# Optimization experiments

Measured on AMD Instinct MI355X. Metric: run time of the kernel, lower is better.

## Reference

```python
import jax, jax.numpy as jnp
import numpy as np

B, C, D = 4096, 1000, 3072


def setup_inputs() -> dict:
    key = jax.random.key(0)
    k1, k2, k3, k4 = jax.random.split(key, 4)
    scale = 1.0
    return {
        "z": jax.random.normal(k1, (B, D), dtype=jnp.float32),
        "sldj": jax.random.normal(k2, (B,), dtype=jnp.float32),
        "labels": jax.random.randint(k3, (B,), 0, C),
        "beta": jnp.ones((), dtype=jnp.float32),
        "means": jax.random.normal(k4, (C, D), dtype=jnp.float32) * scale,
    }


def reference(z, sldj, labels, beta, means):
    # dists[i,j] = -0.5 * ||z_i - mu_j||^2, via a^2 + b^2 - 2ab GEMM trick
    z2 = jnp.sum(z * z, axis=1, keepdims=True)          # [B,1]
    m2 = jnp.sum(means * means, axis=1)[None, :]        # [1,C]
    cross = jnp.einsum('bd,cd->bc', z, means)           # [B,C] GEMM
    dists = -0.5 * (z2 + m2 - 2.0 * cross)              # [B,C]

    log_pz = jax.nn.logsumexp(dists, axis=1)            # [B]
    # cross_entropy(dists, labels) = mean(logsumexp - dists[i, y_i])
    picked = jnp.take_along_axis(dists, labels[:, None], axis=1)[:, 0]
    loss_cls = jnp.mean(log_pz - picked)
    loss_gen = -jnp.mean(log_pz + sldj) / z.shape[1]
    total = loss_gen + beta * loss_cls
    return total, loss_gen, loss_cls
```

## Files before the change

### kernel.cpp

```cpp
#include <hip/hip_runtime.h>
#include <hip/hip_bf16.h>
#include <cstdint>
#include <cstddef>

#define NB 4096
#define NC 1000
#define NCP 1024
#define ND 3072
#define NSL 4
#define KSL (ND / NSL)
#define BM 256
#define BN 256
#define BK 32
#define NT (KSL / BK)
#define ABUF (BM * BK)
#define BBUF (BN * BK)

typedef __attribute__((ext_vector_type(8))) __bf16 bf16x8;
typedef __attribute__((ext_vector_type(4))) float f32x4;
typedef __attribute__((ext_vector_type(4))) unsigned short u16x4;
typedef __attribute__((ext_vector_type(4))) _Float16 f16x4;
typedef unsigned short u16;

__device__ __forceinline__ u16 f2bf_rne(float x) {
    uint32_t u = __float_as_uint(x);
    uint32_t r = (u + 0x7fffu + ((u >> 16) & 1u)) >> 16;
    return (u16)r;
}

__global__ __launch_bounds__(256) void convert_all_kernel(
        const float* __restrict__ z, const float* __restrict__ means,
        u16* __restrict__ zb, u16* __restrict__ mb,
        float* __restrict__ z2, float* __restrict__ m2) {
    const int bidx = blockIdx.x;
    const int tid = threadIdx.x;
    const float* src;
    u16* dst;
    float* sq;
    bool pad = false;
    if (bidx < NB) {
        src = z + (size_t)bidx * ND;
        dst = zb + (size_t)bidx * ND;
        sq = z2 + bidx;
    } else {
        const int mr = bidx - NB;
        dst = mb + (size_t)mr * ND;
        sq = m2 + mr;
        src = means + (size_t)mr * ND;
        pad = (mr >= NC);
    }
    if (!pad) {
        const float4* s = (const float4*)src;
        float acc = 0.f;
#pragma unroll
        for (int i = 0; i < 3; ++i) {
            const int idx = tid + i * 256;
            float4 v = s[idx];
            acc = fmaf(v.x, v.x, acc);
            acc = fmaf(v.y, v.y, acc);
            acc = fmaf(v.z, v.z, acc);
            acc = fmaf(v.w, v.w, acc);
            u16x4 o;
            o.x = f2bf_rne(v.x); o.y = f2bf_rne(v.y);
            o.z = f2bf_rne(v.z); o.w = f2bf_rne(v.w);
            *(u16x4*)(dst + idx * 4) = o;
        }
#pragma unroll
        for (int off = 32; off > 0; off >>= 1) acc += __shfl_xor(acc, off, 64);
        __shared__ float ssum[4];
        const int wid = tid >> 6, lane = tid & 63;
        if (lane == 0) ssum[wid] = acc;
        __syncthreads();
        if (tid == 0) sq[0] = ssum[0] + ssum[1] + ssum[2] + ssum[3];
    } else {
        u16x4 z4 = (u16x4){0, 0, 0, 0};
#pragma unroll
        for (int i = 0; i < 3; ++i) *(u16x4*)(dst + (tid + i * 256) * 4) = z4;
        if (tid == 0) sq[0] = 1e30f;
    }
}

#define GLOAD_LDS16(gp, lp)                                            \
    __builtin_amdgcn_global_load_lds(                                  \
        (const __attribute__((address_space(1))) void*)(gp),           \
        (__attribute__((address_space(3))) void*)(lp), 16, 0, 0)

__global__ __launch_bounds__(1024, 4) void gemm_kernel(
        const u16* __restrict__ zb, const u16* __restrict__ mb,
        _Float16* __restrict__ crossh) {
    __shared__ u16 As[4 * ABUF];
    __shared__ u16 Bs[4 * BBUF];

    const int tid  = threadIdx.x;
    const int wid  = tid >> 6;
    const int lane = tid & 63;
    const int wrr  = (wid >> 2) * 64;
    const int wcc  = (wid & 3) * 64;
    const int lrow = lane & 15;
    const int kgrp = lane >> 4;

    const int bid = blockIdx.x;
    const int w = (bid & 7) * 32 + (bid >> 3);
    const int ksl  = w >> 6;
    const int rem  = w & 63;
    const int brow = (rem >> 2) * BM;
    const int bcol = (rem & 3) * BN;
    const int kbase = ksl * KSL;

    f32x4 acc[4][4];
#pragma unroll
    for (int m = 0; m < 4; ++m)
#pragma unroll
        for (int n = 0; n < 4; ++n) acc[m][n] = (f32x4){0.f, 0.f, 0.f, 0.f};

    const u16* gA;
    const u16* gB;
    u16* lA;
    u16* lB;
    {
        const int r = tid >> 2, p = tid & 3, s = p ^ ((r >> 1) & 3);
        gA = zb + (size_t)(brow + r) * ND + kbase + s * 8;
        gB = mb + (size_t)(bcol + r) * ND + kbase + s * 8;
        lA = As + wid * 512;
        lB = Bs + wid * 512;
    }

#define STAGE(tt) do {                                                   \
        const int bb_ = (tt) & 3;                                        \
        const int ko_ = (tt) * BK;                                       \
        GLOAD_LDS16(gA + ko_, lA + bb_ * ABUF);                          \
        GLOAD_LDS16(gB + ko_, lB + bb_ * BBUF);                          \
    } while (0)

#define COMP(tt) do {                                                    \
        const int cb_ = (tt) & 3;                                        \
        const u16* Ac = As + cb_ * ABUF;                                 \
        const u16* Bc = Bs + cb_ * BBUF;                                 \
        const int pk = kgrp ^ ((lrow >> 1) & 3);                         \
        bf16x8 a0 = *(const bf16x8*)&Ac[(wrr +  0 + lrow) * BK + pk * 8]; \
        bf16x8 a1 = *(const bf16x8*)&Ac[(wrr + 16 + lrow) * BK + pk * 8]; \
        bf16x8 a2 = *(const bf16x8*)&Ac[(wrr + 32 + lrow) * BK + pk * 8]; \
        bf16x8 a3 = *(const bf16x8*)&Ac[(wrr + 48 + lrow) * BK + pk * 8]; \
        _Pragma("unroll")                                                \
        for (int n = 0; n < 4; ++n) {                                    \
            bf16x8 bn = *(const bf16x8*)&Bc[(wcc + n * 16 + lrow) * BK + pk * 8]; \
            acc[0][n] = __builtin_amdgcn_mfma_f32_16x16x32_bf16(a0, bn, acc[0][n], 0, 0, 0); \
            acc[1][n] = __builtin_amdgcn_mfma_f32_16x16x32_bf16(a1, bn, acc[1][n], 0, 0, 0); \
            acc[2][n] = __builtin_amdgcn_mfma_f32_16x16x32_bf16(a2, bn, acc[2][n], 0, 0, 0); \
            acc[3][n] = __builtin_amdgcn_mfma_f32_16x16x32_bf16(a3, bn, acc[3][n], 0, 0, 0); \
        }                                                                \
    } while (0)

    STAGE(0); STAGE(1); STAGE(2);

    for (int t = 0; t < NT - 2; ++t) {
        asm volatile("s_waitcnt vmcnt(4)" ::: "memory");
        __builtin_amdgcn_s_barrier();
        __builtin_amdgcn_sched_barrier(0);
        if (t + 3 < NT) STAGE(t + 3);
        __builtin_amdgcn_sched_barrier(0);
        COMP(t);
    }
    asm volatile("s_waitcnt vmcnt(2)" ::: "memory");
    __builtin_amdgcn_s_barrier();
    __builtin_amdgcn_sched_barrier(0);
    COMP(NT - 2);
    asm volatile("s_waitcnt vmcnt(0)" ::: "memory");
    __builtin_amdgcn_s_barrier();
    __builtin_amdgcn_sched_barrier(0);
    COMP(NT - 1);

#undef STAGE
#undef COMP

    _Float16* outp = crossh + (size_t)ksl * NB * NCP;
#pragma unroll
    for (int n = 0; n < 4; ++n) {
        const int gcol = bcol + wcc + n * 16 + lrow;
#pragma unroll
        for (int m = 0; m < 4; ++m) {
#pragma unroll
            for (int r = 0; r < 4; ++r) {
                const int grow = brow + wrr + m * 16 + kgrp * 4 + r;
                outp[(size_t)grow * NCP + gcol] = (_Float16)acc[m][n][r];
            }
        }
    }
}

__global__ __launch_bounds__(256) void row_lse_kernel(
        const _Float16* __restrict__ crossh, const float* __restrict__ m2,
        const int* __restrict__ labels, const float* __restrict__ sldj,
        float* __restrict__ outA, float* __restrict__ outB) {
    const int row = blockIdx.x;
    const int tid = threadIdx.x;

    float a0 = 0.f, a1 = 0.f, a2 = 0.f, a3 = 0.f;
#pragma unroll
    for (int s = 0; s < NSL; ++s) {
        f16x4 h = ((const f16x4*)(crossh + ((size_t)s * NB + row) * NCP))[tid];
        a0 += (float)h.x; a1 += (float)h.y; a2 += (float)h.z; a3 += (float)h.w;
    }
    float4 mm = ((const float4*)m2)[tid];
    float4 v;
    v.x = a0 - 0.5f * mm.x;
    v.y = a1 - 0.5f * mm.y;
    v.z = a2 - 0.5f * mm.z;
    v.w = a3 - 0.5f * mm.w;

    float mx = fmaxf(fmaxf(v.x, v.y), fmaxf(v.z, v.w));
#pragma unroll
    for (int off = 32; off > 0; off >>= 1) mx = fmaxf(mx, __shfl_xor(mx, off, 64));
    __shared__ float smax[4], ssum[4];
    const int wid = tid >> 6, lane = tid & 63;
    if (lane == 0) smax[wid] = mx;
    __syncthreads();
    const float bm = fmaxf(fmaxf(smax[0], smax[1]), fmaxf(smax[2], smax[3]));

    float s = expf(v.x - bm) + expf(v.y - bm) + expf(v.z - bm) + expf(v.w - bm);
#pragma unroll
    for (int off = 32; off > 0; off >>= 1) s += __shfl_xor(s, off, 64);
    if (lane == 0) ssum[wid] = s;
    __syncthreads();
    if (tid == 0) {
        const float tot = ssum[0] + ssum[1] + ssum[2] + ssum[3];
        const float lpz = bm + logf(tot);
        const int lab = labels[row];
        float pick = 0.f;
#pragma unroll
        for (int si = 0; si < NSL; ++si)
            pick += (float)crossh[((size_t)si * NB + row) * NCP + lab];
        pick -= 0.5f * m2[lab];
        outA[row] = lpz - pick;
        outB[row] = lpz + sldj[row];
    }
}

__global__ __launch_bounds__(1024) void finalize_kernel(
        const float* __restrict__ a, const float* __restrict__ b,
        const float* __restrict__ z2, const float* __restrict__ beta,
        float* __restrict__ out) {
    __shared__ float sa[1024], sb[1024], sz[1024];
    const int tid = threadIdx.x;
    float va = 0.f, vb = 0.f, vz = 0.f;
    for (int i = tid; i < NB; i += 1024) {
        va += a[i]; vb += b[i]; vz += z2[i];
    }
    sa[tid] = va; sb[tid] = vb; sz[tid] = vz;
    __syncthreads();
    for (int s = 512; s > 0; s >>= 1) {
        if (tid < s) {
            sa[tid] += sa[tid + s];
            sb[tid] += sb[tid + s];
            sz[tid] += sz[tid + s];
        }
        __syncthreads();
    }
    if (tid == 0) {
        const float loss_cls = sa[0] / (float)NB;
        const float mean_lpz_sldj = sb[0] / (float)NB - 0.5f * (sz[0] / (float)NB);
        const float loss_gen = -mean_lpz_sldj / (float)ND;
        const float total = loss_gen + beta[0] * loss_cls;
        out[0] = total;
        out[1] = loss_gen;
        out[2] = loss_cls;
    }
}

extern "C" void kernel_launch(void* const* d_in, const int* in_sizes, int n_in,
                              void* d_out, int out_size, void* d_ws, size_t ws_size,
                              hipStream_t stream) {
    const float* z      = (const float*)d_in[0];
    const float* sldj   = (const float*)d_in[1];
    const int*   labels = (const int*)d_in[2];
    const float* beta   = (const float*)d_in[3];
    const float* means  = (const float*)d_in[4];
    float* out = (float*)d_out;

    char* ws = (char*)d_ws;
    size_t off = 0;
    u16* zb = (u16*)(ws + off);           off += (size_t)NB * ND * 2;
    u16* mb = (u16*)(ws + off);           off += (size_t)NCP * ND * 2;
    float* z2 = (float*)(ws + off);       off += (size_t)NB * 4;
    float* m2 = (float*)(ws + off);       off += (size_t)NCP * 4;
    _Float16* crossh = (_Float16*)(ws + off); off += (size_t)NSL * NB * NCP * 2;
    float* ra = (float*)(ws + off);       off += (size_t)NB * 4;
    float* rb = (float*)(ws + off);       off += (size_t)NB * 4;

    convert_all_kernel<<<NB + NCP, 256, 0, stream>>>(z, means, zb, mb, z2, m2);
    gemm_kernel<<<8 * 32 * NSL / 4, 1024, 0, stream>>>(zb, mb, crossh);
    row_lse_kernel<<<NB, 256, 0, stream>>>(crossh, m2, labels, sldj, ra, rb);
    finalize_kernel<<<1, 1024, 0, stream>>>(ra, rb, z2, beta, out);
}
```

Baseline: 60.44 us.

## Halve GEMM threads and give each wave a 128x64 tile for more register reuse

The GEMM block shrinks from 16 waves to 8, and each wave now computes a 128x64 output tile (8x4 MFMA accumulators) instead of 64x64. Each thread issues two global-to-LDS loads per operand per stage, and the vmcnt wait counts are doubled to match. The aim is more MFMAs per LDS fragment read and fewer waves competing for LDS. The MFMA burst is also wrapped in s_setprio. The cost is higher VGPR pressure from 128 accumulator floats per lane and less latency hiding with fewer waves.

```diff
diff --git a/kernel.cpp b/kernel.cpp
--- a/kernel.cpp
+++ b/kernel.cpp
@@ -85,7 +85,7 @@
         (const __attribute__((address_space(1))) void*)(gp),           \
         (__attribute__((address_space(3))) void*)(lp), 16, 0, 0)
 
-__global__ __launch_bounds__(1024, 4) void gemm_kernel(
+__global__ __launch_bounds__(512, 2) void gemm_kernel(
         const u16* __restrict__ zb, const u16* __restrict__ mb,
         _Float16* __restrict__ crossh) {
     __shared__ u16 As[4 * ABUF];
@@ -94,7 +94,7 @@
     const int tid  = threadIdx.x;
     const int wid  = tid >> 6;
     const int lane = tid & 63;
-    const int wrr  = (wid >> 2) * 64;
+    const int wrr  = (wid >> 2) * 128;
     const int wcc  = (wid & 3) * 64;
     const int lrow = lane & 15;
     const int kgrp = lane >> 4;
@@ -107,29 +107,35 @@
     const int bcol = (rem & 3) * BN;
     const int kbase = ksl * KSL;
 
-    f32x4 acc[4][4];
-#pragma unroll
-    for (int m = 0; m < 4; ++m)
+    f32x4 acc[8][4];
+#pragma unroll
+    for (int m = 0; m < 8; ++m)
 #pragma unroll
         for (int n = 0; n < 4; ++n) acc[m][n] = (f32x4){0.f, 0.f, 0.f, 0.f};
 
-    const u16* gA;
-    const u16* gB;
-    u16* lA;
-    u16* lB;
+    const u16* gA0; const u16* gA1; const u16* gB0; const u16* gB1;
+    u16* lA0; u16* lA1; u16* lB0; u16* lB1;
     {
-        const int r = tid >> 2, p = tid & 3, s = p ^ ((r >> 1) & 3);
-        gA = zb + (size_t)(brow + r) * ND + kbase + s * 8;
-        gB = mb + (size_t)(bcol + r) * ND + kbase + s * 8;
-        lA = As + wid * 512;
-        lB = Bs + wid * 512;
+        const int c0 = tid, c1 = tid + 512;
+        const int r0 = c0 >> 2, p0 = c0 & 3, s0 = p0 ^ ((r0 >> 1) & 3);
+        const int r1 = c1 >> 2, p1 = c1 & 3, s1 = p1 ^ ((r1 >> 1) & 3);
+        gA0 = zb + (size_t)(brow + r0) * ND + kbase + s0 * 8;
+        gA1 = zb + (size_t)(brow + r1) * ND + kbase + s1 * 8;
+        gB0 = mb + (size_t)(bcol + r0) * ND + kbase + s0 * 8;
+        gB1 = mb + (size_t)(bcol + r1) * ND + kbase + s1 * 8;
+        lA0 = As + wid * 512;
+        lA1 = As + 4096 + wid * 512;
+        lB0 = Bs + wid * 512;
+        lB1 = Bs + 4096 + wid * 512;
     }
 
 #define STAGE(tt) do {                                                   \
         const int bb_ = (tt) & 3;                                        \
         const int ko_ = (tt) * BK;                                       \
-        GLOAD_LDS16(gA + ko_, lA + bb_ * ABUF);                          \
-        GLOAD_LDS16(gB + ko_, lB + bb_ * BBUF);                          \
+        GLOAD_LDS16(gA0 + ko_, lA0 + bb_ * ABUF);                        \
+        GLOAD_LDS16(gA1 + ko_, lA1 + bb_ * ABUF);                        \
+        GLOAD_LDS16(gB0 + ko_, lB0 + bb_ * BBUF);                        \
+        GLOAD_LDS16(gB1 + ko_, lB1 + bb_ * BBUF);                        \
     } while (0)
 
 #define COMP(tt) do {                                                    \
@@ -137,31 +143,35 @@
         const u16* Ac = As + cb_ * ABUF;                                 \
         const u16* Bc = Bs + cb_ * BBUF;                                 \
         const int pk = kgrp ^ ((lrow >> 1) & 3);                         \
-        bf16x8 a0 = *(const bf16x8*)&Ac[(wrr +  0 + lrow) * BK + pk * 8]; \
-        bf16x8 a1 = *(const bf16x8*)&Ac[(wrr + 16 + lrow) * BK + pk * 8]; \
-        bf16x8 a2 = *(const bf16x8*)&Ac[(wrr + 32 + lrow) * BK + pk * 8]; \
-        bf16x8 a3 = *(const bf16x8*)&Ac[(wrr + 48 + lrow) * BK + pk * 8]; \
+        bf16x8 b[4];                                                     \
         _Pragma("unroll")                                                \
-        for (int n = 0; n < 4; ++n) {                                    \
-            bf16x8 bn = *(const bf16x8*)&Bc[(wcc + n * 16 + lrow) * BK + pk * 8]; \
-            acc[0][n] = __builtin_amdgcn_mfma_f32_16x16x32_bf16(a0, bn, acc[0][n], 0, 0, 0); \
-            acc[1][n] = __builtin_amdgcn_mfma_f32_16x16x32_bf16(a1, bn, acc[1][n], 0, 0, 0); \
-            acc[2][n] = __builtin_amdgcn_mfma_f32_16x16x32_bf16(a2, bn, acc[2][n], 0, 0, 0); \
-            acc[3][n] = __builtin_amdgcn_mfma_f32_16x16x32_bf16(a3, bn, acc[3][n], 0, 0, 0); \
-        }                                                                \
+        for (int n = 0; n < 4; ++n)                                      \
+            b[n] = *(const bf16x8*)&Bc[(wcc + n * 16 + lrow) * BK + pk * 8]; \
+        bf16x8 a[8];                                                     \
+        _Pragma("unroll")                                                \
+        for (int m = 0; m < 8; ++m)                                      \
+            a[m] = *(const bf16x8*)&Ac[(wrr + m * 16 + lrow) * BK + pk * 8]; \
+        __builtin_amdgcn_s_setprio(1);                                   \
+        _Pragma("unroll")                                                \
+        for (int m = 0; m < 8; ++m)                                      \
+            _Pragma("unroll")                                            \
+            for (int n = 0; n < 4; ++n)                                  \
+                acc[m][n] = __builtin_amdgcn_mfma_f32_16x16x32_bf16(     \
+                    a[m], b[n], acc[m][n], 0, 0, 0);                     \
+        __builtin_amdgcn_s_setprio(0);                                   \
     } while (0)
 
     STAGE(0); STAGE(1); STAGE(2);
 
     for (int t = 0; t < NT - 2; ++t) {
-        asm volatile("s_waitcnt vmcnt(4)" ::: "memory");
+        asm volatile("s_waitcnt vmcnt(8)" ::: "memory");
         __builtin_amdgcn_s_barrier();
         __builtin_amdgcn_sched_barrier(0);
         if (t + 3 < NT) STAGE(t + 3);
         __builtin_amdgcn_sched_barrier(0);
         COMP(t);
     }
-    asm volatile("s_waitcnt vmcnt(2)" ::: "memory");
+    asm volatile("s_waitcnt vmcnt(4)" ::: "memory");
     __builtin_amdgcn_s_barrier();
     __builtin_amdgcn_sched_barrier(0);
     COMP(NT - 2);
@@ -178,7 +188,7 @@
     for (int n = 0; n < 4; ++n) {
         const int gcol = bcol + wcc + n * 16 + lrow;
 #pragma unroll
-        for (int m = 0; m < 4; ++m) {
+        for (int m = 0; m < 8; ++m) {
 #pragma unroll
             for (int r = 0; r < 4; ++r) {
                 const int grow = brow + wrr + m * 16 + kgrp * 4 + r;
@@ -288,7 +298,7 @@
     float* rb = (float*)(ws + off);       off += (size_t)NB * 4;
 
     convert_all_kernel<<<NB + NCP, 256, 0, stream>>>(z, means, zb, mb, z2, m2);
-    gemm_kernel<<<8 * 32 * NSL / 4, 1024, 0, stream>>>(zb, mb, crossh);
+    gemm_kernel<<<8 * 32 * NSL / 4, 512, 0, stream>>>(zb, mb, crossh);
     row_lse_kernel<<<NB, 256, 0, stream>>>(crossh, m2, labels, sldj, ra, rb);
     finalize_kernel<<<1, 1024, 0, stream>>>(ra, rb, z2, beta, out);
 }
```

Result: slower. 71.02 us (+17.5%).

## Restructure GEMM into 8-wave, BK=64 quadrant-phased pipeline with double buffering

Applied to the files above, without the earlier changes.

Rewrites the bf16 MFMA GEMM to use 512 threads (8 waves) per 256x256 tile, each wave computing a 128x64 sub-tile. K steps grow to 64 with a double-buffered LDS layout using an XOR swizzle. The loop is split into quadrant phases that interleave global-to-LDS loads with MFMA work, using explicit vmcnt waits and s_setprio. The aim is better load/compute overlap and more data reuse per LDS read, at the cost of higher register pressure and fragile hand-tuned wait counts.

```diff
diff --git a/kernel.cpp b/kernel.cpp
--- a/kernel.cpp
+++ b/kernel.cpp
@@ -11,10 +11,9 @@
 #define KSL (ND / NSL)
 #define BM 256
 #define BN 256
-#define BK 32
-#define NT (KSL / BK)
-#define ABUF (BM * BK)
-#define BBUF (BN * BK)
+#define BKT 64
+#define NKT (KSL / BKT)
+#define TILE (256 * 64)
 
 typedef __attribute__((ext_vector_type(8))) __bf16 bf16x8;
 typedef __attribute__((ext_vector_type(4))) float f32x4;
@@ -85,17 +84,17 @@
         (const __attribute__((address_space(1))) void*)(gp),           \
         (__attribute__((address_space(3))) void*)(lp), 16, 0, 0)
 
-__global__ __launch_bounds__(1024, 4) void gemm_kernel(
+__global__ __launch_bounds__(512, 1) void gemm_kernel(
         const u16* __restrict__ zb, const u16* __restrict__ mb,
         _Float16* __restrict__ crossh) {
-    __shared__ u16 As[4 * ABUF];
-    __shared__ u16 Bs[4 * BBUF];
+    __shared__ u16 As[2 * TILE];
+    __shared__ u16 Bs[2 * TILE];
 
     const int tid  = threadIdx.x;
     const int wid  = tid >> 6;
     const int lane = tid & 63;
-    const int wrr  = (wid >> 2) * 64;
-    const int wcc  = (wid & 3) * 64;
+    const int wm   = wid >> 2;
+    const int wn   = wid & 3;
     const int lrow = lane & 15;
     const int kgrp = lane >> 4;
 
@@ -107,85 +106,133 @@
     const int bcol = (rem & 3) * BN;
     const int kbase = ksl * KSL;
 
-    f32x4 acc[4][4];
-#pragma unroll
-    for (int m = 0; m < 4; ++m)
+    f32x4 acc[8][4];
+#pragma unroll
+    for (int m = 0; m < 8; ++m)
 #pragma unroll
         for (int n = 0; n < 4; ++n) acc[m][n] = (f32x4){0.f, 0.f, 0.f, 0.f};
 
-    const u16* gA;
-    const u16* gB;
-    u16* lA;
-    u16* lB;
-    {
-        const int r = tid >> 2, p = tid & 3, s = p ^ ((r >> 1) & 3);
-        gA = zb + (size_t)(brow + r) * ND + kbase + s * 8;
-        gB = mb + (size_t)(bcol + r) * ND + kbase + s * 8;
-        lA = As + wid * 512;
-        lB = Bs + wid * 512;
-    }
-
-#define STAGE(tt) do {                                                   \
-        const int bb_ = (tt) & 3;                                        \
-        const int ko_ = (tt) * BK;                                       \
-        GLOAD_LDS16(gA + ko_, lA + bb_ * ABUF);                          \
-        GLOAD_LDS16(gB + ko_, lB + bb_ * BBUF);                          \
+    const int l3  = lane >> 3;
+    const int sl8 = ((lane & 7) ^ l3) * 8;
+
+    const u16* gAh[2][2];
+    int AbL[2][2];
+#pragma unroll
+    for (int qm = 0; qm < 2; ++qm)
+#pragma unroll
+        for (int j = 0; j < 2; ++j) {
+            const int r = qm * 64 + j * 128 + wid * 8 + l3;
+            gAh[qm][j] = zb + (size_t)(brow + r) * ND + kbase + sl8;
+            AbL[qm][j] = (qm * 64 + j * 128 + wid * 8) * 64;
+        }
+    const u16* gBh[2][2];
+    int BbL[2][2];
+#pragma unroll
+    for (int qn = 0; qn < 2; ++qn)
+#pragma unroll
+        for (int j = 0; j < 2; ++j) {
+            const int rw0 = j * 64 + wid * 8;
+            const int r0  = (rw0 & 31) + (rw0 >> 5) * 64 + qn * 32;
+            gBh[qn][j] = mb + (size_t)(bcol + r0 + l3) * ND + kbase + sl8;
+            BbL[qn][j] = r0 * 64;
+        }
+
+#define STAGE_A(qm, buf, tt) do {                                        \
+        GLOAD_LDS16(gAh[qm][0] + (tt) * 64, As + (buf) * TILE + AbL[qm][0]); \
+        GLOAD_LDS16(gAh[qm][1] + (tt) * 64, As + (buf) * TILE + AbL[qm][1]); \
     } while (0)
-
-#define COMP(tt) do {                                                    \
-        const int cb_ = (tt) & 3;                                        \
-        const u16* Ac = As + cb_ * ABUF;                                 \
-        const u16* Bc = Bs + cb_ * BBUF;                                 \
-        const int pk = kgrp ^ ((lrow >> 1) & 3);                         \
-        bf16x8 a0 = *(const bf16x8*)&Ac[(wrr +  0 + lrow) * BK + pk * 8]; \
-        bf16x8 a1 = *(const bf16x8*)&Ac[(wrr + 16 + lrow) * BK + pk * 8]; \
-        bf16x8 a2 = *(const bf16x8*)&Ac[(wrr + 32 + lrow) * BK + pk * 8]; \
-        bf16x8 a3 = *(const bf16x8*)&Ac[(wrr + 48 + lrow) * BK + pk * 8]; \
+#define STAGE_B(qn, buf, tt) do {                                        \
+        GLOAD_LDS16(gBh[qn][0] + (tt) * 64, Bs + (buf) * TILE + BbL[qn][0]); \
+        GLOAD_LDS16(gBh[qn][1] + (tt) * 64, Bs + (buf) * TILE + BbL[qn][1]); \
+    } while (0)
+
+#define VM8 asm volatile("s_waitcnt vmcnt(8)" ::: "memory")
+#define VM6 asm volatile("s_waitcnt vmcnt(6)" ::: "memory")
+#define VM4 asm volatile("s_waitcnt vmcnt(4)" ::: "memory")
+#define VM0 asm volatile("s_waitcnt vmcnt(0)" ::: "memory")
+
+#define PHASE(buf, qm, qn, STG, VMW) do {                                \
+        const u16* Ac = As + (buf) * TILE;                               \
+        const u16* Bc = Bs + (buf) * TILE;                               \
+        bf16x8 a[2][4];                                                  \
+        bf16x8 bbf[2][2];                                                \
         _Pragma("unroll")                                                \
-        for (int n = 0; n < 4; ++n) {                                    \
-            bf16x8 bn = *(const bf16x8*)&Bc[(wcc + n * 16 + lrow) * BK + pk * 8]; \
-            acc[0][n] = __builtin_amdgcn_mfma_f32_16x16x32_bf16(a0, bn, acc[0][n], 0, 0, 0); \
-            acc[1][n] = __builtin_amdgcn_mfma_f32_16x16x32_bf16(a1, bn, acc[1][n], 0, 0, 0); \
-            acc[2][n] = __builtin_amdgcn_mfma_f32_16x16x32_bf16(a2, bn, acc[2][n], 0, 0, 0); \
-            acc[3][n] = __builtin_amdgcn_mfma_f32_16x16x32_bf16(a3, bn, acc[3][n], 0, 0, 0); \
+        for (int ks = 0; ks < 2; ++ks) {                                 \
+            const int pk8 = ((ks * 4 + kgrp) ^ (lrow & 7)) * 8;          \
+            _Pragma("unroll")                                            \
+            for (int m = 0; m < 4; ++m)                                  \
+                a[ks][m] = *(const bf16x8*)&Ac[(wm * 128 + (qm) * 64 + m * 16 + lrow) * 64 + pk8]; \
+            _Pragma("unroll")                                            \
+            for (int n = 0; n < 2; ++n)                                  \
+                bbf[ks][n] = *(const bf16x8*)&Bc[(wn * 64 + (qn) * 32 + n * 16 + lrow) * 64 + pk8]; \
         }                                                                \
+        STG;                                                             \
+        __builtin_amdgcn_s_barrier();                                    \
+        asm volatile("s_waitcnt lgkmcnt(0)" ::: "memory");               \
+        __builtin_amdgcn_sched_barrier(0);                               \
+        __builtin_amdgcn_s_setprio(1);                                   \
+        _Pragma("unroll")                                                \
+        for (int ks = 0; ks < 2; ++ks)                                   \
+            _Pragma("unroll")                                            \
+            for (int m = 0; m < 4; ++m)                                  \
+                _Pragma("unroll")                                        \
+                for (int n = 0; n < 2; ++n)                              \
+                    acc[(qm) * 4 + m][(qn) * 2 + n] =                    \
+                        __builtin_amdgcn_mfma_f32_16x16x32_bf16(         \
+                            a[ks][m], bbf[ks][n],                        \
+                            acc[(qm) * 4 + m][(qn) * 2 + n], 0, 0, 0);   \
+        __builtin_amdgcn_s_setprio(0);                                   \
+        VMW;                                                             \
+        __builtin_amdgcn_s_barrier();                                    \
     } while (0)
 
-    STAGE(0); STAGE(1); STAGE(2);
-
-    for (int t = 0; t < NT - 2; ++t) {
-        asm volatile("s_waitcnt vmcnt(4)" ::: "memory");
-        __builtin_amdgcn_s_barrier();
-        __builtin_amdgcn_sched_barrier(0);
-        if (t + 3 < NT) STAGE(t + 3);
-        __builtin_amdgcn_sched_barrier(0);
-        COMP(t);
-    }
-    asm volatile("s_waitcnt vmcnt(2)" ::: "memory");
+    STAGE_A(0, 0, 0); STAGE_B(0, 0, 0);
+    STAGE_A(1, 0, 0); STAGE_B(1, 0, 0);
+    STAGE_A(0, 1, 1); STAGE_B(0, 1, 1);
+    VM8;
     __builtin_amdgcn_s_barrier();
-    __builtin_amdgcn_sched_barrier(0);
-    COMP(NT - 2);
-    asm volatile("s_waitcnt vmcnt(0)" ::: "memory");
-    __builtin_amdgcn_s_barrier();
-    __builtin_amdgcn_sched_barrier(0);
-    COMP(NT - 1);
-
-#undef STAGE
-#undef COMP
+
+    for (int i = 0; i < 5; ++i) {
+        const int ta = 2 * i, tb = 2 * i + 1;
+        PHASE(0, 0, 0, STAGE_A(1, 1, tb),     VM6);
+        PHASE(0, 0, 1, STAGE_B(1, 1, tb),         );
+        PHASE(0, 1, 0, STAGE_A(0, 0, ta + 2),     );
+        PHASE(0, 1, 1, STAGE_B(0, 0, ta + 2), VM8);
+        PHASE(1, 0, 0, STAGE_A(1, 0, ta + 2), VM6);
+        PHASE(1, 0, 1, STAGE_B(1, 0, ta + 2),     );
+        PHASE(1, 1, 0, STAGE_A(0, 1, tb + 2),     );
+        PHASE(1, 1, 1, STAGE_B(0, 1, tb + 2), VM8);
+    }
+    PHASE(0, 0, 0, STAGE_A(1, 1, 11), VM6);
+    PHASE(0, 0, 1, STAGE_B(1, 1, 11),     );
+    PHASE(0, 1, 0, ;,                     );
+    PHASE(0, 1, 1, ;,                 VM4);
+    PHASE(1, 0, 0, ;,                 VM0);
+    PHASE(1, 0, 1, ;,                     );
+    PHASE(1, 1, 0, ;,                     );
+    PHASE(1, 1, 1, ;,                     );
+
+#undef PHASE
+#undef STAGE_A
+#undef STAGE_B
 
     _Float16* outp = crossh + (size_t)ksl * NB * NCP;
 #pragma unroll
-    for (int n = 0; n < 4; ++n) {
-        const int gcol = bcol + wcc + n * 16 + lrow;
-#pragma unroll
-        for (int m = 0; m < 4; ++m) {
-#pragma unroll
-            for (int r = 0; r < 4; ++r) {
-                const int grow = brow + wrr + m * 16 + kgrp * 4 + r;
-                outp[(size_t)grow * NCP + gcol] = (_Float16)acc[m][n][r];
-            }
-        }
-    }
+    for (int qm = 0; qm < 2; ++qm)
+#pragma unroll
+        for (int m = 0; m < 4; ++m)
+#pragma unroll
+            for (int qn = 0; qn < 2; ++qn)
+#pragma unroll
+                for (int n = 0; n < 2; ++n) {
+                    const int gcol = bcol + wn * 64 + qn * 32 + n * 16 + lrow;
+#pragma unroll
+                    for (int r = 0; r < 4; ++r) {
+                        const int grow = brow + wm * 128 + qm * 64 + m * 16 + kgrp * 4 + r;
+                        outp[(size_t)grow * NCP + gcol] =
+                            (_Float16)acc[qm * 4 + m][qn * 2 + n][r];
+                    }
+                }
 }
 
 __global__ __launch_bounds__(256) void row_lse_kernel(
@@ -288,7 +335,7 @@
     float* rb = (float*)(ws + off);       off += (size_t)NB * 4;
 
     convert_all_kernel<<<NB + NCP, 256, 0, stream>>>(z, means, zb, mb, z2, m2);
-    gemm_kernel<<<8 * 32 * NSL / 4, 1024, 0, stream>>>(zb, mb, crossh);
+    gemm_kernel<<<256, 512, 0, stream>>>(zb, mb, crossh);
     row_lse_kernel<<<NB, 256, 0, stream>>>(crossh, m2, labels, sldj, ra, rb);
     finalize_kernel<<<1, 1024, 0, stream>>>(ra, rb, z2, beta, out);
 }
```

Result: slower. 66.55 us (+10.1%).
